# Kernel tuning notes

Measured on AMD Instinct MI355X. Metric: run time of the kernel, lower is better.

The kernel has to match this reference:

```python
import jax, jax.numpy as jnp
import numpy as np

EMBED_DIM = 1024
HEADS = 16
HEAD_DIM = EMBED_DIM // HEADS
N, SEQ = 2, 2048


def setup_inputs() -> dict:
    key = jax.random.key(0)
    ks = jax.random.split(key, 9)
    s = 1.0 / np.sqrt(HEAD_DIM)
    inp = {
        "values": jax.random.normal(ks[0], (N, SEQ, EMBED_DIM), jnp.float32),
        "keys": jax.random.normal(ks[1], (N, SEQ, EMBED_DIM), jnp.float32),
        "query": jax.random.normal(ks[2], (N, SEQ, EMBED_DIM), jnp.float32),
        "mask": jax.random.randint(ks[3], (N, 1, SEQ, SEQ), 0, 2, jnp.int32),
        # per-head projection weights (torch Linear: y = x @ W.T)
        "Wv": jax.random.normal(ks[4], (HEAD_DIM, HEAD_DIM), jnp.float32) * s,
        "Wk": jax.random.normal(ks[5], (HEAD_DIM, HEAD_DIM), jnp.float32) * s,
        "Wq": jax.random.normal(ks[6], (HEAD_DIM, HEAD_DIM), jnp.float32) * s,
        "Wo": jax.random.normal(ks[7], (EMBED_DIM, EMBED_DIM), jnp.float32) * (1.0 / np.sqrt(EMBED_DIM)),
        "bo": jax.random.normal(ks[8], (EMBED_DIM,), jnp.float32) * 0.01,
    }
    return inp


def reference(values, keys, query, mask, Wv, Wk, Wq, Wo, bo):
    n, q_len = query.shape[0], query.shape[1]
    v_len, k_len = values.shape[1], keys.shape[1]
    # reshape to [N, len, H, D]
    v = values.reshape(n, v_len, HEADS, HEAD_DIM)
    k = keys.reshape(n, k_len, HEADS, HEAD_DIM)
    q = query.reshape(n, q_len, HEADS, HEAD_DIM)
    # per-head linear projections (shared weight across heads), torch: x @ W.T
    v = jnp.einsum("nlhd,ed->nlhe", v, Wv)
    k = jnp.einsum("nlhd,ed->nlhe", k, Wk)
    q = jnp.einsum("nlhd,ed->nlhe", q, Wq)
    # energy: [N, H, Q, K]
    energy = jnp.einsum("nqhd,nkhd->nhqk", q, k)
    energy = jnp.where(mask == 0, jnp.float32(-1e20), energy)
    # NOTE: original scales by sqrt(embed_dim), not sqrt(head_dim)
    attention = jax.nn.softmax(energy / jnp.sqrt(jnp.float32(EMBED_DIM)), axis=3)
    out = jnp.einsum("nhql,nlhd->nqhd", attention, v).reshape(n, q_len, EMBED_DIM)
    out = out @ Wo.T + bo  # fc_out; dropout is identity in eval mode
    return out
```

## Files before the change

kernel.cpp:

```cpp
#include <hip/hip_runtime.h>
#include <hip/hip_bf16.h>

#define NB 2
#define SEQ 2048
#define HEADS 16
#define HD 64
#define ED 1024

typedef __bf16 bf16x8 __attribute__((ext_vector_type(8)));
typedef float f32x4 __attribute__((ext_vector_type(4)));
typedef unsigned short u16x8 __attribute__((ext_vector_type(8)));
typedef unsigned short u16x4 __attribute__((ext_vector_type(4)));

#if __has_builtin(__builtin_amdgcn_exp2f)
#define EXP2(x) __builtin_amdgcn_exp2f(x)
#else
#define EXP2(x) __builtin_exp2f(x)
#endif

__device__ __forceinline__ unsigned short f2bf(float f) {
    unsigned u = __builtin_bit_cast(unsigned, f);
    u += 0x7fffu + ((u >> 16) & 1u);
    return (unsigned short)(u >> 16);
}

__device__ __forceinline__ bf16x8 cvt8(const float* __restrict__ p) {
    const float4* p4 = (const float4*)p;
    float4 a = p4[0], b = p4[1];
    u16x8 u;
    u[0] = f2bf(a.x); u[1] = f2bf(a.y); u[2] = f2bf(a.z); u[3] = f2bf(a.w);
    u[4] = f2bf(b.x); u[5] = f2bf(b.y); u[6] = f2bf(b.z); u[7] = f2bf(b.w);
    return __builtin_bit_cast(bf16x8, u);
}

__device__ __forceinline__ bf16x8 ldfrag(const void* p) {
    uint4 v = *(const uint4*)p;
    return __builtin_bit_cast(bf16x8, v);
}

__device__ __forceinline__ f32x4 mfma16(bf16x8 a, bf16x8 b, f32x4 c) {
    return __builtin_amdgcn_mfma_f32_16x16x32_bf16(a, b, c, 0, 0, 0);
}

__device__ __forceinline__ unsigned packbf(float lo, float hi) {
    unsigned a = __builtin_bit_cast(unsigned, hi) + 0x8000u;
    unsigned b = __builtin_bit_cast(unsigned, lo) + 0x8000u;
    return __builtin_amdgcn_perm(a, b, 0x07060302u);
}

#define GLOAD_LDS(gp, lp) \
    __builtin_amdgcn_global_load_lds( \
        (const __attribute__((address_space(1))) unsigned int*)(gp), \
        (__attribute__((address_space(3))) unsigned int*)(lp), 16, 0, 0)

#define QSCALE 0.04508422f

__global__ __launch_bounds__(256) void proj_prep_kernel(
    const float* __restrict__ qin, const float* __restrict__ kin, const float* __restrict__ vin,
    const float* __restrict__ Wq, const float* __restrict__ Wk, const float* __restrict__ Wv,
    unsigned short* __restrict__ Qb, unsigned short* __restrict__ Kb,
    unsigned short* __restrict__ Vt,
    const int* __restrict__ mask, unsigned long long* __restrict__ bits,
    const float* __restrict__ Wo, unsigned short* __restrict__ Wob)
{
    __shared__ __align__(16) char tile[64 * 144];

    int bid = blockIdx.x;
    if (bid >= 3072) {
        int b2 = bid - 3072;
        if (b2 < 2048) {
            int lane = threadIdx.x & 63;
            size_t base = (size_t)b2 * 4096 + (size_t)(threadIdx.x >> 6) * 1024;
#pragma unroll
            for (int j = 0; j < 16; ++j) {
                size_t i = base + (size_t)j * 64 + lane;
                unsigned long long bb = __ballot(mask[i] != 0);
                if (lane == 0) bits[i >> 6] = bb;
            }
        } else {
            size_t i = ((size_t)(b2 - 2048) * 256 + threadIdx.x) * 4;
            float4 v = *(const float4*)(Wo + i);
            u16x4 u;
            u[0] = f2bf(v.x); u[1] = f2bf(v.y); u[2] = f2bf(v.z); u[3] = f2bf(v.w);
            *(u16x4*)(Wob + i) = u;
        }
        return;
    }

    int t3  = bid >> 10;
    int rem = bid & 1023;
    int h   = rem >> 6;
    int rt  = rem & 63;
    int wave = threadIdx.x >> 6, lane = threadIdx.x & 63;
    int quad = lane >> 4, l16 = lane & 15;

    const float* in = (t3 == 0) ? qin : ((t3 == 1) ? kin : vin);
    const float* W  = (t3 == 0) ? Wq  : ((t3 == 1) ? Wk  : Wv);

    int r0 = rt * 64 + wave * 16;

    bf16x8 bf0[4], bf1[4];
#pragma unroll
    for (int sl = 0; sl < 4; ++sl) {
        const float* wrow = W + (sl * 16 + l16) * 64;
        bf0[sl] = cvt8(wrow + quad * 8);
        bf1[sl] = cvt8(wrow + 32 + quad * 8);
    }
    const float* xrow = in + (size_t)(r0 + l16) * ED + h * 64;
    bf16x8 af0 = cvt8(xrow + quad * 8);
    bf16x8 af1 = cvt8(xrow + 32 + quad * 8);

    f32x4 acc[4];
#pragma unroll
    for (int sl = 0; sl < 4; ++sl) {
        f32x4 c = {0.f, 0.f, 0.f, 0.f};
        c = mfma16(af0, bf0[sl], c);
        c = mfma16(af1, bf1[sl], c);
        acc[sl] = c;
    }
    float sc = (t3 == 0) ? QSCALE : 1.0f;

    size_t nh = (size_t)((r0 >> 11) * HEADS + h);
    int rl = lane >> 3, cl = lane & 7;

    if (t3 != 2) {
#pragma unroll
        for (int r = 0; r < 4; ++r) {
            int srow = wave * 16 + quad * 4 + r;
#pragma unroll
            for (int sl = 0; sl < 4; ++sl)
                *(unsigned short*)(tile + srow * 144 + (sl * 16 + l16) * 2) =
                    f2bf(acc[sl][r] * sc);
        }
        unsigned short* dst = (t3 == 0) ? Qb : Kb;
        int s0 = (r0 & 2047);
#pragma unroll
        for (int g = 0; g < 2; ++g) {
            int lrow = wave * 16 + g * 8 + rl;
            uint4 v = *(const uint4*)(tile + lrow * 144 + cl * 16);
            *(uint4*)(dst + (nh * SEQ + (s0 & ~15) + g * 8 + rl) * HD + cl * 8) = v;
        }
    } else {
#pragma unroll
        for (int r = 0; r < 4; ++r) {
            int srow = wave * 16 + quad * 4 + r;
#pragma unroll
            for (int sl = 0; sl < 4; ++sl)
                *(unsigned short*)(tile + (sl * 16 + l16) * 144 + srow * 2) =
                    f2bf(acc[sl][r]);
        }
        __syncthreads();
        int s_tile = rt & 31;
#pragma unroll
        for (int g = 0; g < 2; ++g) {
            int erow = wave * 16 + g * 8 + rl;
            uint4 v = *(const uint4*)(tile + erow * 144 + cl * 16);
            *(uint4*)(Vt + ((nh * 32 + s_tile) * 64 + erow) * 64 + cl * 8) = v;
        }
    }
}

__global__ __launch_bounds__(256, 2) void attn_kernel(
    const unsigned short* __restrict__ Qb, const unsigned short* __restrict__ Kb,
    const unsigned short* __restrict__ Vt2, const unsigned long long* __restrict__ mb,
    unsigned short* __restrict__ Ab)
{
    __shared__ __align__(16) char smem[32768 + 4 * 4096];

    int tid = threadIdx.x;
    int wave = tid >> 6, lane = tid & 63;
    int quad = lane >> 4, l16 = lane & 15;

    int b   = blockIdx.x;
    int xcd = b & 7;
    int j   = b >> 3;
    int nh  = xcd * 4 + (j >> 4);
    int qb  = j & 15;
    int n = nh >> 4, h = nh & 15;
    int q0 = qb * 128 + wave * 16;

    size_t headoff = (size_t)nh * SEQ * HD;
    bf16x8 qf[2][2];
#pragma unroll
    for (int g = 0; g < 2; ++g) {
        const unsigned short* qrow = Qb + headoff + (size_t)(q0 + g * 64 + l16) * HD;
        qf[g][0] = ldfrag(qrow + quad * 8);
        qf[g][1] = ldfrag(qrow + 32 + quad * 8);
    }

    int srow = lane >> 3, sslot = lane & 7;
    int stoff = srow * 128 + (((sslot - srow) & 7) * 16);

    int rotA = ((quad + l16) & 7) * 16;
    int aKV = l16 * 128 + rotA;

    int pswz = (l16 & 7) << 4;
    char* prow0 = smem + 32768 + wave * 4096 + l16 * 128;
    char* prow1 = prow0 + 2048;
    int pwoff = (quad * 8) ^ pswz;
    int proff = (quad * 16) ^ pswz;

    const unsigned short* gK = Kb + headoff;
    const unsigned short* gV = Vt2 + (size_t)nh * (32 * 4096);
    const unsigned long long* mbase = mb + (size_t)n * (SEQ * SEQ / 64)
                                         + (size_t)(q0 + l16) * (SEQ / 64);

    u16x8 ou;
#pragma unroll
    for (int jj = 0; jj < 8; ++jj) ou[jj] = 0x3F80;
    bf16x8 ones = __builtin_bit_cast(bf16x8, ou);

    f32x4 o[2][4] = {};
    f32x4 lacc[2] = {{0,0,0,0},{0,0,0,0}};
    int qsh = quad * 4;

    {
        const char* sK = (const char*)gK + stoff;
        const char* sV = (const char*)gV + stoff;
#pragma unroll
        for (int i2 = 0; i2 < 2; ++i2) {
            int c = wave * 2 + i2;
            GLOAD_LDS(sK + c * 1024, smem + c * 1024);
            GLOAD_LDS(sV + c * 1024, smem + 16384 + c * 1024);
        }
    }
    unsigned long long mnext0 = mbase[0] >> qsh;
    unsigned long long mnext1 = mbase[2048] >> qsh;

    int par = 0;
    for (int kb = 0; kb < SEQ; kb += 64) {
        int kbn = (kb + 64) & (SEQ - 1);
        __syncthreads();
        {
            const char* sK = (const char*)(gK + (size_t)kbn * 64) + stoff;
            const char* sV = (const char*)(gV + (size_t)(kbn >> 6) * 4096) + stoff;
            char* dK = smem + (par ^ 1) * 8192;
            char* dV = smem + 16384 + (par ^ 1) * 8192;
#pragma unroll
            for (int i2 = 0; i2 < 2; ++i2) {
                int c = wave * 2 + i2;
                GLOAD_LDS(sK + c * 1024, dK + c * 1024);
                GLOAD_LDS(sV + c * 1024, dV + c * 1024);
            }
        }
        unsigned long long m64_0 = mnext0, m64_1 = mnext1;
        mnext0 = mbase[kbn >> 6] >> qsh;
        mnext1 = mbase[2048 + (kbn >> 6)] >> qsh;

        const char* kbuf = smem + par * 8192;
        bf16x8 kf[4][2];
#pragma unroll
        for (int kt = 0; kt < 4; ++kt) {
            kf[kt][0] = ldfrag(kbuf + aKV + kt * 2048);
            kf[kt][1] = ldfrag(kbuf + (aKV ^ 64) + kt * 2048);
        }
#pragma unroll
        for (int g = 0; g < 2; ++g) {
            unsigned long long m64 = g ? m64_1 : m64_0;
            char* prow = g ? prow1 : prow0;
            f32x4 c[4];
#pragma unroll
            for (int kt = 0; kt < 4; ++kt) {
                f32x4 cc = {0.f, 0.f, 0.f, 0.f};
                cc = mfma16(kf[kt][0], qf[g][0], cc);
                cc = mfma16(kf[kt][1], qf[g][1], cc);
                c[kt] = cc;
            }
            unsigned mlo = (unsigned)m64;
            unsigned mhi = (unsigned)(m64 >> 32);
#pragma unroll
            for (int kt = 0; kt < 4; ++kt) {
                unsigned mw = (kt & 2) ? mhi : mlo;
                int bs = (kt & 1) ? 16 : 0;
                float p0 = ((mw >> (bs + 0)) & 1u) ? EXP2(c[kt][0]) : 0.f;
                float p1 = ((mw >> (bs + 1)) & 1u) ? EXP2(c[kt][1]) : 0.f;
                float p2 = ((mw >> (bs + 2)) & 1u) ? EXP2(c[kt][2]) : 0.f;
                float p3 = ((mw >> (bs + 3)) & 1u) ? EXP2(c[kt][3]) : 0.f;
                uint2 dw = { packbf(p0, p1), packbf(p2, p3) };
                *(uint2*)(prow + (pwoff ^ (kt * 32))) = dw;
            }
        }
        bf16x8 pb[2][2];
        pb[0][0] = ldfrag(prow0 + proff);
        pb[0][1] = ldfrag(prow0 + (proff ^ 64));
        pb[1][0] = ldfrag(prow1 + proff);
        pb[1][1] = ldfrag(prow1 + (proff ^ 64));
        lacc[0] = mfma16(ones, pb[0][0], lacc[0]);
        lacc[0] = mfma16(ones, pb[0][1], lacc[0]);
        lacc[1] = mfma16(ones, pb[1][0], lacc[1]);
        lacc[1] = mfma16(ones, pb[1][1], lacc[1]);
        const char* vbuf = smem + 16384 + par * 8192;
#pragma unroll
        for (int sl = 0; sl < 4; ++sl) {
            bf16x8 va = ldfrag(vbuf + aKV + sl * 2048);
            bf16x8 vx = ldfrag(vbuf + (aKV ^ 64) + sl * 2048);
            o[0][sl] = mfma16(va, pb[0][0], o[0][sl]);
            o[0][sl] = mfma16(vx, pb[0][1], o[0][sl]);
            o[1][sl] = mfma16(va, pb[1][0], o[1][sl]);
            o[1][sl] = mfma16(vx, pb[1][1], o[1][sl]);
        }
        par ^= 1;
    }

#pragma unroll
    for (int g = 0; g < 2; ++g) {
        float rinv = 1.0f / lacc[g][0];
        int q = q0 + g * 64 + l16;
        unsigned short* op = Ab + (((size_t)(n * SEQ + q)) * HEADS + h) * HD + qsh;
#pragma unroll
        for (int sl = 0; sl < 4; ++sl) {
            u16x4 u;
            u[0] = f2bf(o[g][sl][0] * rinv);
            u[1] = f2bf(o[g][sl][1] * rinv);
            u[2] = f2bf(o[g][sl][2] * rinv);
            u[3] = f2bf(o[g][sl][3] * rinv);
            *(u16x4*)(op + sl * 16) = u;
        }
    }
}

__global__ __launch_bounds__(256) void out_gemm_kernel(
    const unsigned short* __restrict__ Ab, const unsigned short* __restrict__ Wob,
    const float* __restrict__ bo, float* __restrict__ out)
{
    __shared__ __align__(16) char lds[49152];

    int tid = threadIdx.x;
    int wave = tid >> 6, lane = tid & 63;
    int quad = lane >> 4, l16 = lane & 15;
    int bidx = blockIdx.x;
    int xcdg = bidx & 7;
    int jg   = bidx >> 3;
    int rt = xcdg * 4 + (jg & 3);
    int ct = jg >> 2;
    int wr = wave >> 1, wc = wave & 1;

    int srow = lane >> 3, sslot = lane & 7;
    int stoff = srow * 2048 + (((sslot - srow) & 7) * 16);
    const char* gA = (const char*)Ab  + (size_t)rt * 128 * 2048 + stoff;
    const char* gB = (const char*)Wob + (size_t)ct * 64 * 2048 + stoff;

    int aA[4], aB[2];
#pragma unroll
    for (int i = 0; i < 4; ++i) {
        int rowA = wr * 64 + i * 16 + l16;
        aA[i] = rowA * 128 + (((quad + rowA) & 7) * 16);
    }
#pragma unroll
    for (int sl = 0; sl < 2; ++sl) {
        int rowB = wc * 32 + sl * 16 + l16;
        aB[sl] = rowB * 128 + (((quad + rowB) & 7) * 16);
    }

#pragma unroll
    for (int i = 0; i < 4; ++i) {
        int c = wave * 4 + i;
        GLOAD_LDS(gA + (size_t)c * 16384, lds + c * 1024);
    }
#pragma unroll
    for (int i = 0; i < 2; ++i) {
        int c = wave * 2 + i;
        GLOAD_LDS(gB + (size_t)c * 16384, lds + 32768 + c * 1024);
    }

    f32x4 acc[4][2] = {};
    int par = 0;
    for (int f = 0; f < ED; f += 64) {
        int fn = (f + 64) & (ED - 1);
        __syncthreads();
        {
            int pA = (par ^ 1) * 16384;
            int pB = 32768 + (par ^ 1) * 8192;
#pragma unroll
            for (int i = 0; i < 4; ++i) {
                int c = wave * 4 + i;
                GLOAD_LDS(gA + (size_t)c * 16384 + fn * 2, lds + pA + c * 1024);
            }
#pragma unroll
            for (int i = 0; i < 2; ++i) {
                int c = wave * 2 + i;
                GLOAD_LDS(gB + (size_t)c * 16384 + fn * 2, lds + pB + c * 1024);
            }
        }
        int bA = par * 16384;
        int bB = 32768 + par * 8192;
#pragma unroll
        for (int kk = 0; kk < 2; ++kk) {
            int x = kk * 64;
            bf16x8 af[4], bfr[2];
#pragma unroll
            for (int i = 0; i < 4; ++i)    af[i]  = ldfrag(lds + bA + (aA[i] ^ x));
#pragma unroll
            for (int sl = 0; sl < 2; ++sl) bfr[sl] = ldfrag(lds + bB + (aB[sl] ^ x));
#pragma unroll
            for (int i = 0; i < 4; ++i)
#pragma unroll
                for (int sl = 0; sl < 2; ++sl)
                    acc[i][sl] = mfma16(af[i], bfr[sl], acc[i][sl]);
        }
        par ^= 1;
    }

    float bv[2];
#pragma unroll
    for (int sl = 0; sl < 2; ++sl)
        bv[sl] = bo[ct * 64 + wc * 32 + sl * 16 + l16];
#pragma unroll
    for (int i = 0; i < 4; ++i)
#pragma unroll
        for (int r = 0; r < 4; ++r) {
            int row = rt * 128 + wr * 64 + i * 16 + quad * 4 + r;
#pragma unroll
            for (int sl = 0; sl < 2; ++sl) {
                int e = ct * 64 + wc * 32 + sl * 16 + l16;
                out[(size_t)row * ED + e] = acc[i][sl][r] + bv[sl];
            }
        }
}

extern "C" void kernel_launch(void* const* d_in, const int* in_sizes, int n_in,
                              void* d_out, int out_size, void* d_ws, size_t ws_size,
                              hipStream_t stream)
{
    const float* values = (const float*)d_in[0];
    const float* keys   = (const float*)d_in[1];
    const float* query  = (const float*)d_in[2];
    const int*   mask   = (const int*)d_in[3];
    const float* Wv     = (const float*)d_in[4];
    const float* Wk     = (const float*)d_in[5];
    const float* Wq     = (const float*)d_in[6];
    const float* Wo     = (const float*)d_in[7];
    const float* bo     = (const float*)d_in[8];
    float* out = (float*)d_out;

    char* w = (char*)d_ws;
    unsigned short* Qb  = (unsigned short*)(w);
    unsigned short* Kb  = (unsigned short*)(w +  8388608);
    unsigned short* Vt  = (unsigned short*)(w + 16777216);
    unsigned short* Ab  = (unsigned short*)(w + 25165824);
    unsigned long long* Mb = (unsigned long long*)(w + 33554432);
    unsigned short* Wob = (unsigned short*)(w + 34603008);

    proj_prep_kernel<<<3072 + 2048 + 1024, 256, 0, stream>>>(
        query, keys, values, Wq, Wk, Wv, Qb, Kb, Vt, mask, Mb, Wo, Wob);
    attn_kernel<<<512, 256, 0, stream>>>(Qb, Kb, Vt, Mb, Ab);
    out_gemm_kernel<<<512, 256, 0, stream>>>(Ab, Wob, bo, out);
}
```

Baseline: 231.4 us.

## Software-pipeline K fragment loads and stagger K/V prefetch across iterations

Restructures the attention inner loop so the K fragments for the next block are read from LDS into registers before the current PV MFMAs. K is prefetched two blocks ahead and V one block ahead, with the single barrier moved to mid-iteration. The loop is manually unrolled by two with ping-pong register sets, and s_setprio raises wave priority around the MFMA sections. The aim is to hide LDS and global latency behind matrix work, at the cost of more registers and more complex buffer-parity logic.

```diff
diff --git a/kernel.cpp b/kernel.cpp
--- a/kernel.cpp
+++ b/kernel.cpp
@@ -201,7 +201,7 @@
     int proff = (quad * 16) ^ pswz;
 
     const unsigned short* gK = Kb + headoff;
-    const unsigned short* gV = Vt2 + (size_t)nh * (32 * 4096);
+    const char* gV = (const char*)(Vt2 + (size_t)nh * (32 * 4096));
     const unsigned long long* mbase = mb + (size_t)n * (SEQ * SEQ / 64)
                                          + (size_t)(q0 + l16) * (SEQ / 64);
 
@@ -227,33 +227,32 @@
     unsigned long long mnext0 = mbase[0] >> qsh;
     unsigned long long mnext1 = mbase[2048] >> qsh;
 
-    int par = 0;
-    for (int kb = 0; kb < SEQ; kb += 64) {
+    __syncthreads();
+
+    bf16x8 kfA[4][2], kfB[4][2];
+#pragma unroll
+    for (int kt = 0; kt < 4; ++kt) {
+        kfA[kt][0] = ldfrag(smem + aKV + kt * 2048);
+        kfA[kt][1] = ldfrag(smem + (aKV ^ 64) + kt * 2048);
+    }
+    {
+        const char* sK = (const char*)(gK + (size_t)64 * 64) + stoff;
+#pragma unroll
+        for (int i2 = 0; i2 < 2; ++i2) {
+            int c = wave * 2 + i2;
+            GLOAD_LDS(sK + c * 1024, smem + 8192 + c * 1024);
+        }
+    }
+
+    auto body = [&](bf16x8 (&kfc)[4][2], bf16x8 (&kfn)[4][2], int kb, int par) {
         int kbn = (kb + 64) & (SEQ - 1);
-        __syncthreads();
-        {
-            const char* sK = (const char*)(gK + (size_t)kbn * 64) + stoff;
-            const char* sV = (const char*)(gV + (size_t)(kbn >> 6) * 4096) + stoff;
-            char* dK = smem + (par ^ 1) * 8192;
-            char* dV = smem + 16384 + (par ^ 1) * 8192;
-#pragma unroll
-            for (int i2 = 0; i2 < 2; ++i2) {
-                int c = wave * 2 + i2;
-                GLOAD_LDS(sK + c * 1024, dK + c * 1024);
-                GLOAD_LDS(sV + c * 1024, dV + c * 1024);
-            }
-        }
+        int kb2 = (kb + 128) & (SEQ - 1);
         unsigned long long m64_0 = mnext0, m64_1 = mnext1;
         mnext0 = mbase[kbn >> 6] >> qsh;
         mnext1 = mbase[2048 + (kbn >> 6)] >> qsh;
 
-        const char* kbuf = smem + par * 8192;
-        bf16x8 kf[4][2];
-#pragma unroll
-        for (int kt = 0; kt < 4; ++kt) {
-            kf[kt][0] = ldfrag(kbuf + aKV + kt * 2048);
-            kf[kt][1] = ldfrag(kbuf + (aKV ^ 64) + kt * 2048);
-        }
+        bf16x8 pb[2][2];
+        __builtin_amdgcn_s_setprio(1);
 #pragma unroll
         for (int g = 0; g < 2; ++g) {
             unsigned long long m64 = g ? m64_1 : m64_0;
@@ -262,10 +261,11 @@
 #pragma unroll
             for (int kt = 0; kt < 4; ++kt) {
                 f32x4 cc = {0.f, 0.f, 0.f, 0.f};
-                cc = mfma16(kf[kt][0], qf[g][0], cc);
-                cc = mfma16(kf[kt][1], qf[g][1], cc);
+                cc = mfma16(kfc[kt][0], qf[g][0], cc);
+                cc = mfma16(kfc[kt][1], qf[g][1], cc);
                 c[kt] = cc;
             }
+            __builtin_amdgcn_s_setprio(0);
             unsigned mlo = (unsigned)m64;
             unsigned mhi = (unsigned)(m64 >> 32);
 #pragma unroll
@@ -280,7 +280,6 @@
                 *(uint2*)(prow + (pwoff ^ (kt * 32))) = dw;
             }
         }
-        bf16x8 pb[2][2];
         pb[0][0] = ldfrag(prow0 + proff);
         pb[0][1] = ldfrag(prow0 + (proff ^ 64));
         pb[1][0] = ldfrag(prow1 + proff);
@@ -289,7 +288,31 @@
         lacc[0] = mfma16(ones, pb[0][1], lacc[0]);
         lacc[1] = mfma16(ones, pb[1][0], lacc[1]);
         lacc[1] = mfma16(ones, pb[1][1], lacc[1]);
+
+        __syncthreads();
+
+        {
+            const char* kbuf = smem + (par ^ 1) * 8192;
+#pragma unroll
+            for (int kt = 0; kt < 4; ++kt) {
+                kfn[kt][0] = ldfrag(kbuf + aKV + kt * 2048);
+                kfn[kt][1] = ldfrag(kbuf + (aKV ^ 64) + kt * 2048);
+            }
+        }
+        {
+            const char* sK = (const char*)(gK + (size_t)kb2 * 64) + stoff;
+            const char* sV = (const char*)(gV + (size_t)(kbn >> 6) * 8192) + stoff;
+            char* dK = smem + par * 8192;
+            char* dV = smem + 16384 + (par ^ 1) * 8192;
+#pragma unroll
+            for (int i2 = 0; i2 < 2; ++i2) {
+                int c = wave * 2 + i2;
+                GLOAD_LDS(sK + c * 1024, dK + c * 1024);
+                GLOAD_LDS(sV + c * 1024, dV + c * 1024);
+            }
+        }
         const char* vbuf = smem + 16384 + par * 8192;
+        __builtin_amdgcn_s_setprio(1);
 #pragma unroll
         for (int sl = 0; sl < 4; ++sl) {
             bf16x8 va = ldfrag(vbuf + aKV + sl * 2048);
@@ -299,7 +322,12 @@
             o[1][sl] = mfma16(va, pb[1][0], o[1][sl]);
             o[1][sl] = mfma16(vx, pb[1][1], o[1][sl]);
         }
-        par ^= 1;
+        __builtin_amdgcn_s_setprio(0);
+    };
+
+    for (int kb = 0; kb < SEQ; kb += 128) {
+        body(kfA, kfB, kb, 0);
+        body(kfB, kfA, kb + 64, 1);
     }
 
 #pragma unroll
```

Measured after the change: 228.6 us. No clear change (-1.2%).
